# Performance work log

Hardware: AMD Instinct MI355X
Metric: run time of the kernel (lower is better)

The kernel has to match this reference:

```python
import jax, jax.numpy as jnp
import numpy as np

E = 3_200_000
D = 16
N = 100_000


def setup_inputs() -> dict:
    key = jax.random.key(0)
    k1, k2 = jax.random.split(key)
    x = jax.random.normal(k1, (E, D), dtype=jnp.float32)
    edge_dst = jax.random.randint(k2, (E,), 0, N, dtype=jnp.int64)
    return {"x": x, "edge_dst": edge_dst, "num_nodes": N}


def reference(x, edge_dst, num_nodes):
    # sum_over_neighbours: scatter-add edge features to destination atoms -> [N, D]
    summed = jax.ops.segment_sum(x, edge_dst, num_segments=num_nodes)
    # number_of_neighbours(include_central_atom=True): per-atom edge count + 1
    counts = jax.ops.segment_sum(
        jnp.ones((x.shape[0],), dtype=x.dtype), edge_dst, num_segments=num_nodes
    ) + jnp.asarray(1.0, dtype=x.dtype)
    # left_aligned_div by sqrt(counts): broadcast counts over trailing feature dims
    return summed / jnp.sqrt(counts)[:, None]
```

## Files before the change

kernel.cpp:

```cpp
#include <hip/hip_runtime.h>

#define DFEAT 16
#define NPB 64
#define NPB_SHIFT 6
#define EB 8192
#define EB_SHIFT 13
#define BIN_THREADS 1024
#define BATCH (EB / BIN_THREADS)
#define SCAN_BLOCKS 256
#define SCAN_THREADS 256
#define SORT_CAP 3072

__global__ void na_bin_kernel(const int* __restrict__ edge_dst,
                              int* __restrict__ hist,
                              int E, int B, int nblocks) {
    extern __shared__ int h[];
    const int b = blockIdx.x;
    const int t = threadIdx.x;
    for (int i = t; i < B; i += BIN_THREADS) h[i] = 0;
    __syncthreads();
    const int base = b * EB;

    int d[BATCH];
    #pragma unroll
    for (int jj = 0; jj < BATCH; ++jj) {
        int e = base + jj * BIN_THREADS + t;
        d[jj] = (e < E) ? edge_dst[e] : -1;
    }
    #pragma unroll
    for (int jj = 0; jj < BATCH; ++jj)
        if (d[jj] >= 0) atomicAdd(&h[d[jj] >> NPB_SHIFT], 1);

    __syncthreads();
    for (int i = t; i < B; i += BIN_THREADS)
        hist[(size_t)i * nblocks + b] = h[i];
}

__global__ void na_scan_partials(const int* __restrict__ data,
                                 int* __restrict__ blockSums, int M) {
    __shared__ int lds[SCAN_THREADS];
    const int b = blockIdx.x, t = threadIdx.x;
    const int chb = (M + SCAN_BLOCKS - 1) / SCAN_BLOCKS;
    const int bbeg = b * chb;
    const int bend = min(bbeg + chb, M);
    const int cht = (chb + SCAN_THREADS - 1) / SCAN_THREADS;
    const int beg = min(bbeg + t * cht, bend);
    const int end = min(beg + cht, bend);
    int s = 0;
    for (int i = beg; i < end; ++i) s += data[i];
    lds[t] = s;
    __syncthreads();
    for (int off = SCAN_THREADS / 2; off > 0; off >>= 1) {
        if (t < off) lds[t] += lds[t + off];
        __syncthreads();
    }
    if (t == 0) blockSums[b] = lds[0];
}

__global__ void na_scan_blocksums(const int* __restrict__ blockSums,
                                  int* __restrict__ blockOffs) {
    __shared__ int lds[SCAN_BLOCKS];
    const int t = threadIdx.x;
    int v = blockSums[t];
    lds[t] = v;
    __syncthreads();
    for (int off = 1; off < SCAN_BLOCKS; off <<= 1) {
        int add = (t >= off) ? lds[t - off] : 0;
        __syncthreads();
        lds[t] += add;
        __syncthreads();
    }
    blockOffs[t] = lds[t] - v;
}

__global__ void na_scan_final(int* __restrict__ data,
                              const int* __restrict__ blockOffs, int M) {
    __shared__ int lds[SCAN_THREADS];
    const int b = blockIdx.x, t = threadIdx.x;
    const int chb = (M + SCAN_BLOCKS - 1) / SCAN_BLOCKS;
    const int bbeg = b * chb;
    const int bend = min(bbeg + chb, M);
    const int cht = (chb + SCAN_THREADS - 1) / SCAN_THREADS;
    const int beg = min(bbeg + t * cht, bend);
    const int end = min(beg + cht, bend);
    int s = 0;
    for (int i = beg; i < end; ++i) s += data[i];
    lds[t] = s;
    __syncthreads();
    for (int off = 1; off < SCAN_THREADS; off <<= 1) {
        int add = (t >= off) ? lds[t - off] : 0;
        __syncthreads();
        lds[t] += add;
        __syncthreads();
    }
    int run = blockOffs[b] + lds[t] - s;
    for (int i = beg; i < end; ++i) {
        int c = data[i];
        data[i] = run;
        run += c;
    }
}

__global__ void na_scatter_fused(const int* __restrict__ edge_dst,
                                 const int* __restrict__ offs,
                                 int* __restrict__ binned,
                                 int E, int B, int nblocks) {
    extern __shared__ int h[];
    const int b = blockIdx.x;
    const int t = threadIdx.x;
    for (int i = t; i < B; i += BIN_THREADS)
        h[i] = offs[(size_t)i * nblocks + b];
    __syncthreads();
    const int base = b * EB;

    int d[BATCH];
    #pragma unroll
    for (int jj = 0; jj < BATCH; ++jj) {
        int e = base + jj * BIN_THREADS + t;
        d[jj] = (e < E) ? edge_dst[e] : -1;
    }
    #pragma unroll
    for (int jj = 0; jj < BATCH; ++jj) {
        if (d[jj] >= 0) {
            int n = d[jj];
            int e = base + jj * BIN_THREADS + t;
            int pos = atomicAdd(&h[n >> NPB_SHIFT], 1);
            binned[pos] = ((n & (NPB - 1)) << 22) | e;
        }
    }
}

__global__ __launch_bounds__(256, 7)
void na_sort_gather(const float* __restrict__ x,
                    const int* __restrict__ binned,
                    const int* __restrict__ offs,
                    float* __restrict__ out,
                    int E, int N, int B, int nblocks) {
    __shared__ int sorted[SORT_CAP];
    __shared__ int cnt[NPB];
    __shared__ int cur[NPB];
    __shared__ int excl[NPB + 1];

    const int k = blockIdx.x;
    const int t = threadIdx.x;

    const int beg = offs[(size_t)k * nblocks];
    const int end = (k + 1 < B) ? offs[(size_t)(k + 1) * nblocks] : E;
    const int sz = end - beg;

    if (t < NPB) { cnt[t] = 0; cur[t] = 0; }
    __syncthreads();

    if (sz <= SORT_CAP) {
        for (int j = t; j < sz; j += 256)
            atomicAdd(&cnt[binned[beg + j] >> 22], 1);
        __syncthreads();
        if (t < 64) {
            int v = cnt[t];
            int inc = v;
            #pragma unroll
            for (int d = 1; d < 64; d <<= 1) {
                int u = __shfl_up(inc, d);
                if (t >= d) inc += u;
            }
            excl[t] = inc - v;
            if (t == 63) excl[NPB] = inc;
        }
        __syncthreads();
        for (int j = t; j < sz; j += 256) {
            int v = binned[beg + j];
            int d = v >> 22;
            int r = atomicAdd(&cur[d], 1);
            sorted[excl[d] + r] = v & 0x3FFFFF;
        }
        __syncthreads();

        const int g = t >> 4;
        const int lane16 = t & 15;
        const int es = lane16 >> 2;
        const int q = lane16 & 3;
        const float4* x4 = reinterpret_cast<const float4*>(x);

        for (int ln = g; ln < NPB; ln += 16) {
            int n = k * NPB + ln;
            if (n >= N) break;
            int lbeg = excl[ln], lend = excl[ln + 1];
            float ax = 0.f, ay = 0.f, az = 0.f, aw = 0.f;

            int i = lbeg + es;
            for (; i + 12 < lend; i += 16) {
                int e0 = sorted[i];
                int e1 = sorted[i + 4];
                int e2 = sorted[i + 8];
                int e3 = sorted[i + 12];
                float4 v0 = x4[(size_t)e0 * 4 + q];
                float4 v1 = x4[(size_t)e1 * 4 + q];
                float4 v2 = x4[(size_t)e2 * 4 + q];
                float4 v3 = x4[(size_t)e3 * 4 + q];
                ax += (v0.x + v1.x) + (v2.x + v3.x);
                ay += (v0.y + v1.y) + (v2.y + v3.y);
                az += (v0.z + v1.z) + (v2.z + v3.z);
                aw += (v0.w + v1.w) + (v2.w + v3.w);
            }
            for (; i < lend; i += 4) {
                int e0 = sorted[i];
                float4 v0 = x4[(size_t)e0 * 4 + q];
                ax += v0.x; ay += v0.y; az += v0.z; aw += v0.w;
            }

            ax += __shfl_xor(ax, 4); ay += __shfl_xor(ay, 4);
            az += __shfl_xor(az, 4); aw += __shfl_xor(aw, 4);
            ax += __shfl_xor(ax, 8); ay += __shfl_xor(ay, 8);
            az += __shfl_xor(az, 8); aw += __shfl_xor(aw, 8);

            float s = rsqrtf((float)(lend - lbeg) + 1.0f);
            if (es == 0) {
                float4 r; r.x = ax * s; r.y = ay * s; r.z = az * s; r.w = aw * s;
                reinterpret_cast<float4*>(out)[(size_t)n * 4 + q] = r;
            }
        }
    } else {
        const int ln = t >> 2;
        const int q = t & 3;
        const float4* x4 = reinterpret_cast<const float4*>(x);
        int n = k * NPB + ln;
        if (n < N) {
            float ax = 0.f, ay = 0.f, az = 0.f, aw = 0.f;
            int deg = 0;
            for (int j = 0; j < sz; ++j) {
                int v = binned[beg + j];
                if ((v >> 22) == ln) {
                    float4 vv = x4[(size_t)(v & 0x3FFFFF) * 4 + q];
                    ax += vv.x; ay += vv.y; az += vv.z; aw += vv.w;
                    ++deg;
                }
            }
            float s = rsqrtf((float)deg + 1.0f);
            float4 r; r.x = ax * s; r.y = ay * s; r.z = az * s; r.w = aw * s;
            reinterpret_cast<float4*>(out)[(size_t)n * 4 + q] = r;
        }
    }
}

extern "C" void kernel_launch(void* const* d_in, const int* in_sizes, int n_in,
                              void* d_out, int out_size, void* d_ws, size_t ws_size,
                              hipStream_t stream) {
    const float* x        = (const float*)d_in[0];
    const int*   edge_dst = (const int*)d_in[1];
    float*       out      = (float*)d_out;

    const int E = in_sizes[1];
    const int N = out_size / DFEAT;
    const int B = (N + NPB - 1) >> NPB_SHIFT;
    const int nblocks = (E + EB - 1) >> EB_SHIFT;
    const int M = B * nblocks;

    int* binned    = (int*)d_ws;
    int* hist      = binned + E;
    int* blockSums = hist + M;
    int* blockOffs = blockSums + SCAN_BLOCKS;

    na_bin_kernel<<<nblocks, BIN_THREADS, B * sizeof(int), stream>>>(
        edge_dst, hist, E, B, nblocks);
    na_scan_partials<<<SCAN_BLOCKS, SCAN_THREADS, 0, stream>>>(hist, blockSums, M);
    na_scan_blocksums<<<1, SCAN_BLOCKS, 0, stream>>>(blockSums, blockOffs);
    na_scan_final<<<SCAN_BLOCKS, SCAN_THREADS, 0, stream>>>(hist, blockOffs, M);
    na_scatter_fused<<<nblocks, BIN_THREADS, B * sizeof(int), stream>>>(
        edge_dst, hist, binned, E, B, nblocks);
    na_sort_gather<<<B, 256, 0, stream>>>(x, binned, hist, out, E, N, B, nblocks);
}
```

Before: 129.7 us.

## Replace three-pass global scan with per-bucket row scan plus bucket base scan

The flat three-kernel scan over the bucket-by-block histogram is replaced by a per-bucket row scan (one 64-thread wavefront per bucket, using shuffles) and a single-block scan over the bucket totals. Scatter and sort-gather then combine the bucket base with the row offset. The binning block size is also doubled to 16384 edges with 512 threads, processed in chunks of 8 loads, which halves the number of histogram columns. The aim is to remove one launch and the strided global scan, at the cost of a serial single-block scan over about 1563 buckets and fewer, larger binning blocks.

After: 120.4 us (median of 2 runs). 1.08x faster.

```diff
diff --git a/kernel.cpp b/kernel.cpp
--- a/kernel.cpp
+++ b/kernel.cpp
@@ -3,12 +3,9 @@
 #define DFEAT 16
 #define NPB 64
 #define NPB_SHIFT 6
-#define EB 8192
-#define EB_SHIFT 13
-#define BIN_THREADS 1024
+#define EB 16384
+#define BIN_THREADS 512
 #define BATCH (EB / BIN_THREADS)
-#define SCAN_BLOCKS 256
-#define SCAN_THREADS 256
 #define SORT_CAP 3072
 
 __global__ void na_bin_kernel(const int* __restrict__ edge_dst,
@@ -21,111 +18,106 @@
     __syncthreads();
     const int base = b * EB;
 
-    int d[BATCH];
     #pragma unroll
-    for (int jj = 0; jj < BATCH; ++jj) {
-        int e = base + jj * BIN_THREADS + t;
-        d[jj] = (e < E) ? edge_dst[e] : -1;
-    }
-    #pragma unroll
-    for (int jj = 0; jj < BATCH; ++jj)
-        if (d[jj] >= 0) atomicAdd(&h[d[jj] >> NPB_SHIFT], 1);
-
+    for (int c = 0; c < BATCH; c += 8) {
+        int d[8];
+        #pragma unroll
+        for (int jj = 0; jj < 8; ++jj) {
+            int e = base + (c + jj) * BIN_THREADS + t;
+            d[jj] = (e < E) ? edge_dst[e] : -1;
+        }
+        #pragma unroll
+        for (int jj = 0; jj < 8; ++jj)
+            if (d[jj] >= 0) atomicAdd(&h[d[jj] >> NPB_SHIFT], 1);
+    }
     __syncthreads();
     for (int i = t; i < B; i += BIN_THREADS)
         hist[(size_t)i * nblocks + b] = h[i];
 }
 
-__global__ void na_scan_partials(const int* __restrict__ data,
-                                 int* __restrict__ blockSums, int M) {
-    __shared__ int lds[SCAN_THREADS];
-    const int b = blockIdx.x, t = threadIdx.x;
-    const int chb = (M + SCAN_BLOCKS - 1) / SCAN_BLOCKS;
-    const int bbeg = b * chb;
-    const int bend = min(bbeg + chb, M);
-    const int cht = (chb + SCAN_THREADS - 1) / SCAN_THREADS;
-    const int beg = min(bbeg + t * cht, bend);
-    const int end = min(beg + cht, bend);
+__global__ void na_row_scan(int* __restrict__ hist,
+                            int* __restrict__ bucketTotal,
+                            int nblocks) {
+    const int k = blockIdx.x;
+    const int t = threadIdx.x;
+    int* row = hist + (size_t)k * nblocks;
+    const int CPT = (nblocks + 63) >> 6;
+    const int beg = min(t * CPT, nblocks);
+    const int end = min(beg + CPT, nblocks);
+
     int s = 0;
-    for (int i = beg; i < end; ++i) s += data[i];
+    for (int i = beg; i < end; ++i) s += row[i];
+    int inc = s;
+    #pragma unroll
+    for (int d = 1; d < 64; d <<= 1) {
+        int u = __shfl_up(inc, d);
+        if (t >= d) inc += u;
+    }
+    int run = inc - s;
+    for (int i = beg; i < end; ++i) {
+        int c = row[i];
+        row[i] = run;
+        run += c;
+    }
+    if (t == 63) bucketTotal[k] = inc;
+}
+
+__global__ void na_base_scan(const int* __restrict__ bucketTotal,
+                             int* __restrict__ bucketBase,
+                             int B) {
+    __shared__ int lds[1024];
+    const int t = threadIdx.x;
+    const int CPT = (B + 1023) >> 10;
+    const int beg = min(t * CPT, B);
+    const int end = min(beg + CPT, B);
+    int s = 0;
+    for (int i = beg; i < end; ++i) s += bucketTotal[i];
     lds[t] = s;
     __syncthreads();
-    for (int off = SCAN_THREADS / 2; off > 0; off >>= 1) {
-        if (t < off) lds[t] += lds[t + off];
-        __syncthreads();
-    }
-    if (t == 0) blockSums[b] = lds[0];
-}
-
-__global__ void na_scan_blocksums(const int* __restrict__ blockSums,
-                                  int* __restrict__ blockOffs) {
-    __shared__ int lds[SCAN_BLOCKS];
-    const int t = threadIdx.x;
-    int v = blockSums[t];
-    lds[t] = v;
-    __syncthreads();
-    for (int off = 1; off < SCAN_BLOCKS; off <<= 1) {
+    for (int off = 1; off < 1024; off <<= 1) {
         int add = (t >= off) ? lds[t - off] : 0;
         __syncthreads();
         lds[t] += add;
         __syncthreads();
     }
-    blockOffs[t] = lds[t] - v;
-}
-
-__global__ void na_scan_final(int* __restrict__ data,
-                              const int* __restrict__ blockOffs, int M) {
-    __shared__ int lds[SCAN_THREADS];
-    const int b = blockIdx.x, t = threadIdx.x;
-    const int chb = (M + SCAN_BLOCKS - 1) / SCAN_BLOCKS;
-    const int bbeg = b * chb;
-    const int bend = min(bbeg + chb, M);
-    const int cht = (chb + SCAN_THREADS - 1) / SCAN_THREADS;
-    const int beg = min(bbeg + t * cht, bend);
-    const int end = min(beg + cht, bend);
-    int s = 0;
-    for (int i = beg; i < end; ++i) s += data[i];
-    lds[t] = s;
-    __syncthreads();
-    for (int off = 1; off < SCAN_THREADS; off <<= 1) {
-        int add = (t >= off) ? lds[t - off] : 0;
-        __syncthreads();
-        lds[t] += add;
-        __syncthreads();
-    }
-    int run = blockOffs[b] + lds[t] - s;
+    int run = lds[t] - s;
     for (int i = beg; i < end; ++i) {
-        int c = data[i];
-        data[i] = run;
+        int c = bucketTotal[i];
+        bucketBase[i] = run;
         run += c;
     }
+    if (t == 1023) bucketBase[B] = lds[1023];
 }
 
 __global__ void na_scatter_fused(const int* __restrict__ edge_dst,
-                                 const int* __restrict__ offs,
+                                 const int* __restrict__ hist,
+                                 const int* __restrict__ bucketBase,
                                  int* __restrict__ binned,
                                  int E, int B, int nblocks) {
     extern __shared__ int h[];
     const int b = blockIdx.x;
     const int t = threadIdx.x;
     for (int i = t; i < B; i += BIN_THREADS)
-        h[i] = offs[(size_t)i * nblocks + b];
+        h[i] = bucketBase[i] + hist[(size_t)i * nblocks + b];
     __syncthreads();
     const int base = b * EB;
 
-    int d[BATCH];
     #pragma unroll
-    for (int jj = 0; jj < BATCH; ++jj) {
-        int e = base + jj * BIN_THREADS + t;
-        d[jj] = (e < E) ? edge_dst[e] : -1;
-    }
-    #pragma unroll
-    for (int jj = 0; jj < BATCH; ++jj) {
-        if (d[jj] >= 0) {
-            int n = d[jj];
-            int e = base + jj * BIN_THREADS + t;
-            int pos = atomicAdd(&h[n >> NPB_SHIFT], 1);
-            binned[pos] = ((n & (NPB - 1)) << 22) | e;
+    for (int c = 0; c < BATCH; c += 8) {
+        int d[8];
+        #pragma unroll
+        for (int jj = 0; jj < 8; ++jj) {
+            int e = base + (c + jj) * BIN_THREADS + t;
+            d[jj] = (e < E) ? edge_dst[e] : -1;
+        }
+        #pragma unroll
+        for (int jj = 0; jj < 8; ++jj) {
+            if (d[jj] >= 0) {
+                int n = d[jj];
+                int e = base + (c + jj) * BIN_THREADS + t;
+                int pos = atomicAdd(&h[n >> NPB_SHIFT], 1);
+                binned[pos] = ((n & (NPB - 1)) << 22) | e;
+            }
         }
     }
 }
@@ -133,9 +125,9 @@
 __global__ __launch_bounds__(256, 7)
 void na_sort_gather(const float* __restrict__ x,
                     const int* __restrict__ binned,
-                    const int* __restrict__ offs,
+                    const int* __restrict__ bucketBase,
                     float* __restrict__ out,
-                    int E, int N, int B, int nblocks) {
+                    int N) {
     __shared__ int sorted[SORT_CAP];
     __shared__ int cnt[NPB];
     __shared__ int cur[NPB];
@@ -144,8 +136,8 @@
     const int k = blockIdx.x;
     const int t = threadIdx.x;
 
-    const int beg = offs[(size_t)k * nblocks];
-    const int end = (k + 1 < B) ? offs[(size_t)(k + 1) * nblocks] : E;
+    const int beg = bucketBase[k];
+    const int end = bucketBase[k + 1];
     const int sz = end - beg;
 
     if (t < NPB) { cnt[t] = 0; cur[t] = 0; }
@@ -252,20 +244,19 @@
     const int E = in_sizes[1];
     const int N = out_size / DFEAT;
     const int B = (N + NPB - 1) >> NPB_SHIFT;
-    const int nblocks = (E + EB - 1) >> EB_SHIFT;
+    const int nblocks = (E + EB - 1) / EB;
     const int M = B * nblocks;
 
-    int* binned    = (int*)d_ws;
-    int* hist      = binned + E;
-    int* blockSums = hist + M;
-    int* blockOffs = blockSums + SCAN_BLOCKS;
+    int* binned      = (int*)d_ws;
+    int* hist        = binned + E;
+    int* bucketTotal = hist + M;
+    int* bucketBase  = bucketTotal + B;
 
     na_bin_kernel<<<nblocks, BIN_THREADS, B * sizeof(int), stream>>>(
         edge_dst, hist, E, B, nblocks);
-    na_scan_partials<<<SCAN_BLOCKS, SCAN_THREADS, 0, stream>>>(hist, blockSums, M);
-    na_scan_blocksums<<<1, SCAN_BLOCKS, 0, stream>>>(blockSums, blockOffs);
-    na_scan_final<<<SCAN_BLOCKS, SCAN_THREADS, 0, stream>>>(hist, blockOffs, M);
+    na_row_scan<<<B, 64, 0, stream>>>(hist, bucketTotal, nblocks);
+    na_base_scan<<<1, 1024, 0, stream>>>(bucketTotal, bucketBase, B);
     na_scatter_fused<<<nblocks, BIN_THREADS, B * sizeof(int), stream>>>(
-        edge_dst, hist, binned, E, B, nblocks);
-    na_sort_gather<<<B, 256, 0, stream>>>(x, binned, hist, out, E, N, B, nblocks);
-}
+        edge_dst, hist, bucketBase, binned, E, B, nblocks);
+    na_sort_gather<<<B, 256, 0, stream>>>(x, binned, bucketBase, out, N);
+}
```
